# Performance work log

Measured on AMD Instinct MI355X. Metric: run time of the kernel, lower is better.

The kernel has to match this reference:

```python
import jax, jax.numpy as jnp
import numpy as np

B, C, N = 2, 512, 2048
HEADS, DIM_HEAD, SCALE = 16, 64, 8.0
H_DIM = HEADS * DIM_HEAD
EPS = 1e-12  # F.normalize default eps


def setup_inputs() -> dict:
    key = jax.random.key(0)
    ks = jax.random.split(key, 5)
    x = jax.random.normal(ks[0], (B, C, N), dtype=jnp.float32)
    Wqkv = jax.random.normal(ks[1], (3 * H_DIM, C), dtype=jnp.float32) * (1.0 / np.sqrt(C))
    q_scale = jnp.ones((DIM_HEAD,), dtype=jnp.float32)
    k_scale = jnp.ones((DIM_HEAD,), dtype=jnp.float32)
    Wout = jax.random.normal(ks[2], (C, H_DIM), dtype=jnp.float32) * (1.0 / np.sqrt(H_DIM))
    bout = jax.random.normal(ks[3], (C,), dtype=jnp.float32) * 0.01
    return {"x": x, "Wqkv": Wqkv, "q_scale": q_scale, "k_scale": k_scale,
            "Wout": Wout, "bout": bout}


def _l2norm(t):
    # F.normalize(t, dim=-1): t / max(||t||, eps)
    n = jnp.sqrt(jnp.sum(t * t, axis=-1, keepdims=True))
    return t / jnp.maximum(n, EPS)


def reference(x, Wqkv, q_scale, k_scale, Wout, bout):
    # 1x1 conv == pointwise matmul over channel dim
    qkv = jnp.einsum('oc,bcn->bon', Wqkv, x)              # [B, 3*H_DIM, N]
    q, k, v = jnp.split(qkv, 3, axis=1)
    # unflatten channels -> [B, H, D, N]
    def to_heads(t):
        return t.reshape(B, HEADS, DIM_HEAD, N)
    q, k, v = map(to_heads, (q, k, v))
    # cosine attention: l2-normalize q,k over head dim, apply learned per-dim scales
    q = _l2norm(q.transpose(0, 1, 3, 2)) * q_scale        # [B, H, N, D]
    k = _l2norm(k.transpose(0, 1, 3, 2)) * k_scale        # [B, H, N, D]
    sim = jnp.einsum('bhid,bhjd->bhij', q, k) * SCALE     # [B, H, N, N]
    attn = jax.nn.softmax(sim, axis=-1)
    out = jnp.einsum('bhij,bhdj->bhid', attn, v)          # [B, H, N, D]
    out = out.transpose(0, 1, 3, 2).reshape(B, H_DIM, N)  # b h n d -> b (h d) n
    return jnp.einsum('oc,bcn->bon', Wout, out) + bout[None, :, None]
```

## Files before the change

kernel.cpp:

```cpp
#include <hip/hip_runtime.h>
#include <hip/hip_bf16.h>

#define BATCH 2
#define CCH   512
#define NSEQ  2048
#define HEADS 16
#define DHEAD 64
#define HDIM  1024
#define ODIM  3072
#define QK_PRESCALE 11.541560327111707f

typedef short short4v __attribute__((ext_vector_type(4)));
typedef short short8 __attribute__((ext_vector_type(8)));
typedef float float4v __attribute__((ext_vector_type(4)));
typedef int   int4v   __attribute__((ext_vector_type(4)));

__device__ __forceinline__ unsigned short f2bf(float f) {
    unsigned int u = __float_as_uint(f);
    return (unsigned short)((u + 0x7FFFu + ((u >> 16) & 1u)) >> 16);
}
__device__ __forceinline__ unsigned short f2bf_fast(float f) {
    return (unsigned short)((__float_as_uint(f) + 0x8000u) >> 16);
}
__device__ __forceinline__ float fexp2(float x) {
#if __has_builtin(__builtin_amdgcn_exp2f)
    return __builtin_amdgcn_exp2f(x);
#else
    return exp2f(x);
#endif
}
__device__ __forceinline__ int pack_bf16(float lo, float hi) {
#if __has_builtin(__builtin_amdgcn_cvt_pk_bf16_f32)
    typedef __bf16 bf2_t __attribute__((ext_vector_type(2)));
    bf2_t v = __builtin_amdgcn_cvt_pk_bf16_f32(lo, hi);
    return __builtin_bit_cast(int, v);
#else
    return (int)f2bf_fast(lo) | ((int)(unsigned)f2bf_fast(hi) << 16);
#endif
}

typedef __attribute__((address_space(1))) const void* as1_cvp;
typedef __attribute__((address_space(3))) void* as3_vp;
__device__ __forceinline__ void cp16(const void* g, void* l) {
    __builtin_amdgcn_global_load_lds((as1_cvp)g, (as3_vp)l, 16, 0, 0);
}
__global__ __launch_bounds__(256) void k_prep(
    const float* __restrict__ Wqkv, const float* __restrict__ Wout,
    const float* __restrict__ x,
    const float* __restrict__ qs, const float* __restrict__ ks,
    unsigned short* __restrict__ Wqkvb, unsigned short* __restrict__ Woutb,
    unsigned short* __restrict__ xt, float* __restrict__ M) {
    const int bx = blockIdx.x;
    if (bx < 2048) {
        if (bx == 0 && threadIdx.x < 64) {
            int lane = threadIdx.x;
            float p = fabsf(qs[lane] * ks[lane]);
#pragma unroll
            for (int off = 1; off < 64; off <<= 1) p = fmaxf(p, __shfl_xor(p, off));
            if (lane == 0) *M = QK_PRESCALE * p;
        }
        int i4 = (bx * 256 + threadIdx.x) * 4;
        const float* src; unsigned short* dst; int idx;
        if (i4 < ODIM * CCH) { src = Wqkv; dst = Wqkvb; idx = i4; }
        else { src = Wout; dst = Woutb; idx = i4 - ODIM * CCH; }
        float4 v = *(const float4*)(src + idx);
        ushort4 o;
        o.x = f2bf(v.x); o.y = f2bf(v.y); o.z = f2bf(v.z); o.w = f2bf(v.w);
        *(ushort4*)(dst + idx) = o;
        return;
    }
    __shared__ unsigned short t[64][65];
    const int fx = bx - 2048;
    const int n0 = (fx & 31) * 64;
    const int c0 = ((fx >> 5) & 7) * 64;
    const int b  = fx >> 8;
    const int tr = threadIdx.x >> 6, tc = threadIdx.x & 63;
    const float* xs = x + (size_t)b * CCH * NSEQ;
    unsigned short* xd = xt + (size_t)b * NSEQ * CCH;
#pragma unroll
    for (int r = 0; r < 16; ++r) {
        int c = r * 4 + tr;
        t[c][tc] = f2bf(xs[(size_t)(c0 + c) * NSEQ + n0 + tc]);
    }
    __syncthreads();
#pragma unroll
    for (int r = 0; r < 16; ++r) {
        int n = r * 4 + tr;
        xd[(size_t)(n0 + n) * CCH + c0 + tc] = t[tc][n];
    }
}

__global__ __launch_bounds__(256) void k_gemm_qkv(
    const unsigned short* __restrict__ W, const unsigned short* __restrict__ xt,
    const float* __restrict__ qs, const float* __restrict__ ks,
    unsigned short* __restrict__ qh, unsigned short* __restrict__ kh,
    unsigned short* __restrict__ vb) {
    constexpr int K = CCH, N = NSEQ;
    __shared__ __align__(16) short smem[2 * 2 * 128 * 32];
    const int tid = threadIdx.x, wave = tid >> 6, lane = tid & 63;
    const int l15 = lane & 15, quad = lane >> 4;
    const int n0 = blockIdx.x * 128, m0 = blockIdx.y * 128, z = blockIdx.z;
    const short* Ab = (const short*)W + (size_t)m0 * K;
    const short* Bb = (const short*)xt + ((size_t)z * N + n0) * K;
    const int wm = wave >> 1, wn = wave & 1;
    const int srow = tid >> 2;
    const int cswz2 = (((tid & 3) ^ ((srow >> 1) & 3))) * 8;
    const int rchunk = ((quad ^ ((l15 >> 1) & 3))) * 8;

    float4v acc[4][4];
#pragma unroll
    for (int i = 0; i < 4; ++i)
#pragma unroll
        for (int j = 0; j < 4; ++j) acc[i][j] = (float4v){0.f, 0.f, 0.f, 0.f};

#define STAGEQ(K0_, BUF_) do {                                                   \
        short* bA = smem + (BUF_) * 8192 + wave * 512;                           \
        cp16(Ab + (size_t)srow * K + (K0_) + cswz2, bA);                         \
        cp16(Ab + (size_t)(64 + srow) * K + (K0_) + cswz2, bA + 2048);           \
        cp16(Bb + (size_t)srow * K + (K0_) + cswz2, bA + 4096);                  \
        cp16(Bb + (size_t)(64 + srow) * K + (K0_) + cswz2, bA + 6144);           \
    } while (0)

    STAGEQ(0, 0);
    __syncthreads();
    for (int ksi = 0; ksi < K / 32; ++ksi) {
        const int rb = ksi & 1;
        if (ksi + 1 < K / 32) STAGEQ((ksi + 1) * 32, rb ^ 1);
        const short* sA = smem + rb * 8192;
        const short* sB = sA + 4096;
        short8 af[4], bfr[4];
#pragma unroll
        for (int t = 0; t < 4; ++t) {
            af[t]  = *(const short8*)&sA[(wm * 64 + t * 16 + l15) * 32 + rchunk];
            bfr[t] = *(const short8*)&sB[(wn * 64 + t * 16 + l15) * 32 + rchunk];
        }
#pragma unroll
        for (int mt = 0; mt < 4; ++mt)
#pragma unroll
            for (int nt = 0; nt < 4; ++nt)
                acc[mt][nt] = __builtin_amdgcn_mfma_f32_16x16x32_bf16(af[mt], bfr[nt], acc[mt][nt], 0, 0, 0);
        __syncthreads();
    }
#undef STAGEQ

    const int co   = (m0 + wm * 64) >> 6;
    const int part = co >> 4;
    const int h    = co & 15;
    const int bh   = z * HEADS + h;
    short* myT = smem + wave * 4096;

    if (part < 2) {
        float inv[4];
#pragma unroll
        for (int nt = 0; nt < 4; ++nt) {
            float ss = 0.f;
#pragma unroll
            for (int mt = 0; mt < 4; ++mt)
#pragma unroll
                for (int r = 0; r < 4; ++r) ss += acc[mt][nt][r] * acc[mt][nt][r];
            ss += __shfl_xor(ss, 16);
            ss += __shfl_xor(ss, 32);
            inv[nt] = 1.0f / fmaxf(sqrtf(ss), 1e-12f);
        }
        const float* sc = part ? ks : qs;
        const float csc = part ? 1.0f : QK_PRESCALE;
#pragma unroll
        for (int mt = 0; mt < 4; ++mt) {
            const int db = mt * 16 + quad * 4;
            float4 s4 = *(const float4*)(sc + db);
            s4.x *= csc; s4.y *= csc; s4.z *= csc; s4.w *= csc;
#pragma unroll
            for (int nt = 0; nt < 4; ++nt) {
                int nl = nt * 16 + l15;
                short4v o;
                o.x = (short)f2bf(acc[mt][nt][0] * inv[nt] * s4.x);
                o.y = (short)f2bf(acc[mt][nt][1] * inv[nt] * s4.y);
                o.z = (short)f2bf(acc[mt][nt][2] * inv[nt] * s4.z);
                o.w = (short)f2bf(acc[mt][nt][3] * inv[nt] * s4.w);
                *(short4v*)&myT[nl * 64 + (((db >> 3) ^ (nl & 7)) << 3) + (db & 7)] = o;
            }
        }
        unsigned short* dst = (part ? kh : qh) + (size_t)bh * NSEQ * DHEAD
                              + (size_t)(n0 + wn * 64) * DHEAD;
#pragma unroll
        for (int pass = 0; pass < 8; ++pass) {
            int nl = pass * 8 + (lane >> 3), c = lane & 7;
            short8 vv = *(const short8*)&myT[nl * 64 + ((c ^ (nl & 7)) << 3)];
            *(short8*)&dst[(size_t)nl * DHEAD + c * 8] = vv;
        }
    } else {
#pragma unroll
        for (int mt = 0; mt < 4; ++mt)
#pragma unroll
            for (int nt = 0; nt < 4; ++nt) {
                int nl = nt * 16 + l15;
                int swc = nl >> 3, swo = nl & 7;
#pragma unroll
                for (int r = 0; r < 4; ++r) {
                    int d = mt * 16 + quad * 4 + r;
                    myT[d * 64 + ((swc ^ (d & 7)) << 3) + swo] = (short)f2bf(acc[mt][nt][r]);
                }
            }
        unsigned short* dst = vb + (size_t)bh * DHEAD * NSEQ + n0 + wn * 64;
#pragma unroll
        for (int pass = 0; pass < 8; ++pass) {
            int d = pass * 8 + (lane >> 3), c = lane & 7;
            short8 vv = *(const short8*)&myT[d * 64 + ((c ^ (d & 7)) << 3)];
            *(short8*)&dst[(size_t)d * NSEQ + c * 8] = vv;
        }
    }
}

#define KVB 32
__global__ __launch_bounds__(512, 4) void k_attn(
    const unsigned short* __restrict__ qh, const unsigned short* __restrict__ kh,
    const unsigned short* __restrict__ vb,
    unsigned short* __restrict__ aot, const float* __restrict__ Mptr) {
    __shared__ __align__(16) short Kt[2][4][KVB * 64];
    __shared__ __align__(16) short Vt[2][4][64 * KVB];
    const int tid = threadIdx.x, wave = tid >> 6, lane = tid & 63;
    const int grp = wave >> 2, w4 = wave & 3;
    const int gtid = tid & 255;
    const int l15 = lane & 15, quad = lane >> 4, q8 = quad * 8;
    const int flat = blockIdx.x;
    const int xcd = flat & 7, idx = flat >> 3;
    const int bh = xcd * 4 + (idx >> 4);
    const int i0 = (idx & 15) * 128;
    const int b = bh >> 4, h = bh & 15;
    const float Ms = *Mptr;
    const float4v mInit = (float4v){-Ms, -Ms, -Ms, -Ms};
    const int srow = gtid >> 3;
    const int kkey  = (srow & 3) | (((srow >> 3) & 1) << 2);
    const int cswzK = ((gtid & 7) ^ kkey) * 8;
    const int srowV = gtid >> 2;
    const int cswzV = ((gtid & 3) ^ ((srowV >> 1) & 3)) * 8;
    const int ksw = l15 & 7;
    const int kc0 = ((0 + quad) ^ ksw) * 8;
    const int kc1 = ((4 + quad) ^ ksw) * 8;
    const int vkr = (l15 >> 1) & 3;
    const int ar0 = (l15 >> 2) * 8 + (l15 & 3);
    const int ar1 = ar0 + 4;
    const int jbase = grp * (NSEQ / 2);

    short8 qf[2][2];
    {
        const short* qb = (const short*)qh + ((size_t)bh * NSEQ + i0 + w4 * 32) * DHEAD;
#pragma unroll
        for (int it = 0; it < 2; ++it) {
            qf[it][0] = *(const short8*)&qb[(it * 16 + l15) * DHEAD + q8];
            qf[it][1] = *(const short8*)&qb[(it * 16 + l15) * DHEAD + 32 + q8];
        }
    }

    float4v of[2][4];
#pragma unroll
    for (int it = 0; it < 2; ++it)
#pragma unroll
        for (int dt = 0; dt < 4; ++dt) of[it][dt] = (float4v){0.f, 0.f, 0.f, 0.f};
    float l_acc[2] = {0.f, 0.f};

    const short* kbase = (const short*)kh + ((size_t)bh * NSEQ + jbase) * DHEAD;
    const short* vbase = (const short*)vb + (size_t)bh * DHEAD * NSEQ + jbase;

#define STAGE(T_, B_) do {                                                       \
        cp16(kbase + (size_t)((T_) * KVB + srow) * DHEAD + cswzK,                \
             &Kt[grp][B_][w4 * 512]);                                            \
        cp16(vbase + (size_t)srowV * NSEQ + (T_) * KVB + cswzV,                  \
             &Vt[grp][B_][w4 * 512]);                                            \
    } while (0)

#define COMPUTE(CB_) do {                                                        \
        const short* Kb = &Kt[grp][CB_][0];                                      \
        const short* Vb = &Vt[grp][CB_][0];                                      \
        __builtin_amdgcn_s_setprio(1);                                           \
        short8 av[4];                                                            \
        _Pragma("unroll")                                                        \
        for (int dt = 0; dt < 4; ++dt)                                           \
            av[dt] = *(const short8*)&Vb[(dt * 16 + l15) * KVB + ((quad ^ vkr) * 8)]; \
        int4v pw[2];                                                             \
        _Pragma("unroll")                                                        \
        for (int t2 = 0; t2 < 2; ++t2) {                                         \
            const int arow = t2 ? ar1 : ar0;                                     \
            const short* kr = &Kb[arow * 64];                                    \
            short8 kf0 = *(const short8*)&kr[kc0];                               \
            short8 kf1 = *(const short8*)&kr[kc1];                               \
            _Pragma("unroll")                                                    \
            for (int it = 0; it < 2; ++it) {                                     \
                float4v s = mInit;                                               \
                s = __builtin_amdgcn_mfma_f32_16x16x32_bf16(kf0, qf[it][0], s, 0, 0, 0); \
                s = __builtin_amdgcn_mfma_f32_16x16x32_bf16(kf1, qf[it][1], s, 0, 0, 0); \
                float p0 = fexp2(s[0]);                                          \
                float p1 = fexp2(s[1]);                                          \
                float p2 = fexp2(s[2]);                                          \
                float p3 = fexp2(s[3]);                                          \
                l_acc[it] += (p0 + p1) + (p2 + p3);                              \
                pw[it][t2 * 2 + 0] = pack_bf16(p0, p1);                          \
                pw[it][t2 * 2 + 1] = pack_bf16(p2, p3);                          \
            }                                                                    \
        }                                                                        \
        {                                                                        \
            short8 pb0 = __builtin_bit_cast(short8, pw[0]);                      \
            short8 pb1 = __builtin_bit_cast(short8, pw[1]);                      \
            _Pragma("unroll")                                                    \
            for (int dt = 0; dt < 4; ++dt) {                                     \
                of[0][dt] = __builtin_amdgcn_mfma_f32_16x16x32_bf16(av[dt], pb0, of[0][dt], 0, 0, 0); \
                of[1][dt] = __builtin_amdgcn_mfma_f32_16x16x32_bf16(av[dt], pb1, of[1][dt], 0, 0, 0); \
            }                                                                    \
        }                                                                        \
        __builtin_amdgcn_s_setprio(0);                                           \
    } while (0)

#define WAITBAR(N_) do {                                                         \
        asm volatile("s_waitcnt vmcnt(" #N_ ")" ::: "memory");                   \
        __builtin_amdgcn_s_barrier();                                            \
        __builtin_amdgcn_sched_barrier(0);                                       \
    } while (0)

    constexpr int T = (NSEQ / 2) / KVB;
    STAGE(0, 0);
    STAGE(1, 1);
    for (int t = 0; t < T - 2; ++t) {
        STAGE(t + 2, (t + 2) & 3);
        WAITBAR(4);
        COMPUTE(t & 3);
    }
    WAITBAR(2);
    COMPUTE((T - 2) & 3);
    WAITBAR(0);
    COMPUTE((T - 1) & 3);
#undef STAGE
#undef COMPUTE
#undef WAITBAR

    float lred[2];
#pragma unroll
    for (int it = 0; it < 2; ++it) {
        float l = l_acc[it];
        l += __shfl_xor(l, 16);
        l += __shfl_xor(l, 32);
        lred[it] = l;
    }

    __syncthreads();

    float* F = (float*)&Kt[0][0][0];
    float* L = (float*)&Vt[0][0][0];
    if (grp == 1) {
#pragma unroll
        for (int it = 0; it < 2; ++it) {
#pragma unroll
            for (int dt = 0; dt < 4; ++dt)
                *(float4v*)&F[(((w4 * 2 + it) * 4 + dt) * 64 + lane) * 4] = of[it][dt];
            L[(w4 * 2 + it) * 64 + lane] = lred[it];
        }
    }
    __syncthreads();
    if (grp == 0) {
#pragma unroll
        for (int it = 0; it < 2; ++it) {
            float lt = lred[it] + L[(w4 * 2 + it) * 64 + lane];
            float inv = 1.0f / fmaxf(lt, 1e-30f);
            unsigned short* ob = aot + ((size_t)b * NSEQ + i0 + w4 * 32 + it * 16 + l15) * HDIM + h * DHEAD;
#pragma unroll
            for (int dt = 0; dt < 4; ++dt) {
                float4v p = *(const float4v*)&F[(((w4 * 2 + it) * 4 + dt) * 64 + lane) * 4];
                ushort4 o;
                o.x = f2bf((of[it][dt][0] + p[0]) * inv);
                o.y = f2bf((of[it][dt][1] + p[1]) * inv);
                o.z = f2bf((of[it][dt][2] + p[2]) * inv);
                o.w = f2bf((of[it][dt][3] + p[3]) * inv);
                *(ushort4*)&ob[dt * 16 + quad * 4] = o;
            }
        }
    }
}

__global__ __launch_bounds__(256) void k_gemm_out(
    const unsigned short* __restrict__ W, const unsigned short* __restrict__ aot,
    const float* __restrict__ bias, float* __restrict__ out) {
    constexpr int K = HDIM, N = NSEQ, M = CCH;
    __shared__ __align__(16) short lsm[2 * 2 * 64 * 64];
    const int tid = threadIdx.x, wave = tid >> 6, lane = tid & 63;
    const int l15 = lane & 15, quad = lane >> 4;
    const int n0 = blockIdx.x * 64, m0 = blockIdx.y * 64, z = blockIdx.z;
    const short* Ab = (const short*)W + (size_t)m0 * K;
    const short* Bb = (const short*)aot + ((size_t)z * N + n0) * K;
    const int wm = wave >> 1, wn = wave & 1;
    const int srow = tid >> 3;
    const int cswz = (((tid & 7) ^ (srow & 7))) * 8;
    const int sw7 = (l15 & 7);

    float4v acc[2][2];
#pragma unroll
    for (int i = 0; i < 2; ++i)
#pragma unroll
        for (int j = 0; j < 2; ++j) acc[i][j] = (float4v){0.f, 0.f, 0.f, 0.f};

#define STAGEO(K0_, BUF_) do {                                                   \
        short* bA = lsm + (BUF_) * 8192 + wave * 512;                            \
        cp16(Ab + (size_t)srow * K + (K0_) + cswz, bA);                          \
        cp16(Ab + (size_t)(srow + 32) * K + (K0_) + cswz, bA + 2048);            \
        cp16(Bb + (size_t)srow * K + (K0_) + cswz, bA + 4096);                   \
        cp16(Bb + (size_t)(srow + 32) * K + (K0_) + cswz, bA + 6144);            \
    } while (0)

    STAGEO(0, 0);
    __syncthreads();
    for (int ksi = 0; ksi < K / 64; ++ksi) {
        const int rb = ksi & 1;
        if (ksi + 1 < K / 64) STAGEO((ksi + 1) * 64, rb ^ 1);
        const short* sA = lsm + rb * 8192;
        const short* sB = sA + 4096;
        short8 af[2][2], bfr[2][2];
#pragma unroll
        for (int t = 0; t < 2; ++t)
#pragma unroll
            for (int kk = 0; kk < 2; ++kk) {
                af[t][kk]  = *(const short8*)&sA[(wm * 32 + t * 16 + l15) * 64 + ((kk * 4 + quad) ^ sw7) * 8];
                bfr[t][kk] = *(const short8*)&sB[(wn * 32 + t * 16 + l15) * 64 + ((kk * 4 + quad) ^ sw7) * 8];
            }
#pragma unroll
        for (int mt = 0; mt < 2; ++mt)
#pragma unroll
            for (int nt = 0; nt < 2; ++nt) {
                acc[mt][nt] = __builtin_amdgcn_mfma_f32_16x16x32_bf16(af[mt][0], bfr[nt][0], acc[mt][nt], 0, 0, 0);
                acc[mt][nt] = __builtin_amdgcn_mfma_f32_16x16x32_bf16(af[mt][1], bfr[nt][1], acc[mt][nt], 0, 0, 0);
            }
        __syncthreads();
    }
#undef STAGEO
    float* Co = out + (size_t)z * M * N;
#pragma unroll
    for (int mt = 0; mt < 2; ++mt)
#pragma unroll
        for (int nt = 0; nt < 2; ++nt) {
            int mrow = m0 + wm * 32 + mt * 16 + quad * 4;
#pragma unroll
            for (int r = 0; r < 4; ++r) {
                int mr = mrow + r;
                int nc = n0 + wn * 32 + nt * 16 + l15;
                Co[(size_t)mr * N + nc] = acc[mt][nt][r] + bias[mr];
            }
        }
}

extern "C" void kernel_launch(void* const* d_in, const int* in_sizes, int n_in,
                              void* d_out, int out_size, void* d_ws, size_t ws_size,
                              hipStream_t stream) {
    const float* x = nullptr; const float* Wqkv = nullptr;
    const float* qs = nullptr; const float* ks = nullptr;
    const float* Wout = nullptr; const float* bout = nullptr;
    for (int i = 0; i < n_in; ++i) {
        switch (in_sizes[i]) {
            case BATCH * CCH * NSEQ: x    = (const float*)d_in[i]; break;
            case ODIM * CCH:         Wqkv = (const float*)d_in[i]; break;
            case CCH * HDIM:         Wout = (const float*)d_in[i]; break;
            case CCH:                bout = (const float*)d_in[i]; break;
            case DHEAD: if (!qs) qs = (const float*)d_in[i]; else ks = (const float*)d_in[i]; break;
            default: break;
        }
    }
    float* y = (float*)d_out;

    char* ws = (char*)d_ws;
    float*          Mbuf  = (float*)(ws + 0);
    unsigned short* Wqkvb = (unsigned short*)(ws + 4096);
    unsigned short* Woutb = (unsigned short*)(ws + 3149824);
    unsigned short* xt    = (unsigned short*)(ws + 4198400);
    unsigned short* qh    = (unsigned short*)(ws + 8392704);
    unsigned short* kh    = (unsigned short*)(ws + 16781312);
    unsigned short* vb    = (unsigned short*)(ws + 25169920);
    unsigned short* aot   = (unsigned short*)(ws + 33558528);

    k_prep<<<dim3(2048 + 512), 256, 0, stream>>>(Wqkv, Wout, x, qs, ks, Wqkvb, Woutb, xt, Mbuf);
    k_gemm_qkv<<<dim3(NSEQ / 128, ODIM / 128, BATCH), 256, 0, stream>>>(Wqkvb, xt, qs, ks, qh, kh, vb);
    k_attn<<<dim3(512), 512, 0, stream>>>(qh, kh, vb, aot, Mbuf);
    k_gemm_out<<<dim3(NSEQ / 64, CCH / 64, BATCH), 256, 0, stream>>>(Woutb, aot, bout, y);
}
```

Before: 142.2 us.

## Fuse all four stages into one cooperative persistent kernel with grid syncs

Replaces the four separate launches (prep, QKV GEMM, attention, output GEMM) with a single cooperative kernel of 512 blocks of 512 threads, separated by grid.sync barriers. Each block's two 256-thread halves take on the prep and GEMM tiles that previously ran as separate blocks, and the original multi-launch path is kept as a fallback if the cooperative launch fails. This removes launch gaps and per-kernel tail effects, at the cost of fixed block counts: the output GEMM uses only half the threads, and some QKV tiles sit idle in one half.

```diff
diff --git a/kernel.cpp b/kernel.cpp
--- a/kernel.cpp
+++ b/kernel.cpp
@@ -1,5 +1,8 @@
 #include <hip/hip_runtime.h>
 #include <hip/hip_bf16.h>
+#include <hip/hip_cooperative_groups.h>
+
+namespace cg = cooperative_groups;
 
 #define BATCH 2
 #define CCH   512
@@ -444,6 +447,439 @@
         }
 }
 
+__global__ __launch_bounds__(512, 4) void k_fused(
+    const float* __restrict__ Wqkv, const float* __restrict__ Wout,
+    const float* __restrict__ x,
+    const float* __restrict__ qs, const float* __restrict__ ks,
+    unsigned short* __restrict__ Wqkvb, unsigned short* __restrict__ Woutb,
+    unsigned short* __restrict__ xt, float* __restrict__ Mbuf,
+    unsigned short* __restrict__ qh, unsigned short* __restrict__ kh,
+    unsigned short* __restrict__ vb, unsigned short* __restrict__ aot,
+    const float* __restrict__ bout, float* __restrict__ y) {
+    __shared__ __align__(16) short SMEM[32768];
+    cg::grid_group grid = cg::this_grid();
+    const int tid = threadIdx.x;
+    const int rb = blockIdx.x;
+    const int hf = tid >> 8;
+    const int t256 = tid & 255;
+
+    {
+        unsigned short* tt = (unsigned short*)(SMEM + hf * 16384);
+        const int s = rb * 2 + hf;
+        for (int k = 0; k < 3; ++k) {
+            const int v = s + k * 1024;
+            const bool a = v < 2560;
+            if (a && v < 2048) {
+                if (v == 0 && t256 < 64) {
+                    int lane = t256;
+                    float p = fabsf(qs[lane] * ks[lane]);
+#pragma unroll
+                    for (int off = 1; off < 64; off <<= 1) p = fmaxf(p, __shfl_xor(p, off));
+                    if (lane == 0) *Mbuf = QK_PRESCALE * p;
+                }
+                int i4 = (v * 256 + t256) * 4;
+                const float* src; unsigned short* dst; int idx;
+                if (i4 < ODIM * CCH) { src = Wqkv; dst = Wqkvb; idx = i4; }
+                else { src = Wout; dst = Woutb; idx = i4 - ODIM * CCH; }
+                float4 vv = *(const float4*)(src + idx);
+                ushort4 o;
+                o.x = f2bf(vv.x); o.y = f2bf(vv.y); o.z = f2bf(vv.z); o.w = f2bf(vv.w);
+                *(ushort4*)(dst + idx) = o;
+            }
+            const int fx = v - 2048;
+            const int tr = t256 >> 6, tc = t256 & 63;
+            if (a && v >= 2048) {
+                const int n0 = (fx & 31) * 64;
+                const int c0 = ((fx >> 5) & 7) * 64;
+                const int b  = fx >> 8;
+                const float* xs = x + (size_t)b * CCH * NSEQ;
+#pragma unroll
+                for (int r = 0; r < 16; ++r) {
+                    int c = r * 4 + tr;
+                    tt[c * 65 + tc] = f2bf(xs[(size_t)(c0 + c) * NSEQ + n0 + tc]);
+                }
+            }
+            __syncthreads();
+            if (a && v >= 2048) {
+                const int n0 = (fx & 31) * 64;
+                const int c0 = ((fx >> 5) & 7) * 64;
+                const int b  = fx >> 8;
+                unsigned short* xd = xt + (size_t)b * NSEQ * CCH;
+#pragma unroll
+                for (int r = 0; r < 16; ++r) {
+                    int n = r * 4 + tr;
+                    xd[(size_t)(n0 + n) * CCH + c0 + tc] = tt[tc * 65 + n];
+                }
+            }
+            __syncthreads();
+        }
+    }
+    grid.sync();
+
+    {
+        const int s = rb * 2 + hf;
+        bool act; int v;
+        if (s < 512)      { act = true;  v = s; }
+        else if (hf == 0) { act = true;  v = 512 + (rb - 256); }
+        else              { act = false; v = 0; }
+        constexpr int K = CCH, N = NSEQ;
+        short* smq = SMEM + hf * 16384;
+        const int wave = t256 >> 6, lane = t256 & 63;
+        const int l15 = lane & 15, quad = lane >> 4;
+        const int z = v / 384, rr = v % 384;
+        const int m0 = (rr >> 4) * 128, n0 = (rr & 15) * 128;
+        const short* Ab = (const short*)Wqkvb + (size_t)m0 * K;
+        const short* Bb = (const short*)xt + ((size_t)z * N + n0) * K;
+        const int wm = wave >> 1, wn = wave & 1;
+        const int srow = t256 >> 2;
+        const int cswz2 = (((t256 & 3) ^ ((srow >> 1) & 3))) * 8;
+        const int rchunk = ((quad ^ ((l15 >> 1) & 3))) * 8;
+
+        float4v acc[4][4];
+#pragma unroll
+        for (int i = 0; i < 4; ++i)
+#pragma unroll
+            for (int j = 0; j < 4; ++j) acc[i][j] = (float4v){0.f, 0.f, 0.f, 0.f};
+
+#define FQ_STAGE(K0_, BUF_) do {                                                 \
+        short* bA = smq + (BUF_) * 8192 + wave * 512;                            \
+        cp16(Ab + (size_t)srow * K + (K0_) + cswz2, bA);                         \
+        cp16(Ab + (size_t)(64 + srow) * K + (K0_) + cswz2, bA + 2048);           \
+        cp16(Bb + (size_t)srow * K + (K0_) + cswz2, bA + 4096);                  \
+        cp16(Bb + (size_t)(64 + srow) * K + (K0_) + cswz2, bA + 6144);           \
+    } while (0)
+
+        if (act) FQ_STAGE(0, 0);
+        __syncthreads();
+        for (int ksi = 0; ksi < K / 32; ++ksi) {
+            if (act) {
+                const int pb = ksi & 1;
+                if (ksi + 1 < K / 32) FQ_STAGE((ksi + 1) * 32, pb ^ 1);
+                const short* sA = smq + pb * 8192;
+                const short* sB = sA + 4096;
+                short8 af[4], bfr[4];
+#pragma unroll
+                for (int t = 0; t < 4; ++t) {
+                    af[t]  = *(const short8*)&sA[(wm * 64 + t * 16 + l15) * 32 + rchunk];
+                    bfr[t] = *(const short8*)&sB[(wn * 64 + t * 16 + l15) * 32 + rchunk];
+                }
+#pragma unroll
+                for (int mt = 0; mt < 4; ++mt)
+#pragma unroll
+                    for (int nt = 0; nt < 4; ++nt)
+                        acc[mt][nt] = __builtin_amdgcn_mfma_f32_16x16x32_bf16(af[mt], bfr[nt], acc[mt][nt], 0, 0, 0);
+            }
+            __syncthreads();
+        }
+#undef FQ_STAGE
+
+        if (act) {
+            const int co   = (m0 + wm * 64) >> 6;
+            const int part = co >> 4;
+            const int h    = co & 15;
+            const int bh   = z * HEADS + h;
+            short* myT = smq + wave * 4096;
+
+            if (part < 2) {
+                float inv[4];
+#pragma unroll
+                for (int nt = 0; nt < 4; ++nt) {
+                    float ss = 0.f;
+#pragma unroll
+                    for (int mt = 0; mt < 4; ++mt)
+#pragma unroll
+                        for (int r = 0; r < 4; ++r) ss += acc[mt][nt][r] * acc[mt][nt][r];
+                    ss += __shfl_xor(ss, 16);
+                    ss += __shfl_xor(ss, 32);
+                    inv[nt] = 1.0f / fmaxf(sqrtf(ss), 1e-12f);
+                }
+                const float* sc = part ? ks : qs;
+                const float csc = part ? 1.0f : QK_PRESCALE;
+#pragma unroll
+                for (int mt = 0; mt < 4; ++mt) {
+                    const int db = mt * 16 + quad * 4;
+                    float4 s4 = *(const float4*)(sc + db);
+                    s4.x *= csc; s4.y *= csc; s4.z *= csc; s4.w *= csc;
+#pragma unroll
+                    for (int nt = 0; nt < 4; ++nt) {
+                        int nl = nt * 16 + l15;
+                        short4v o;
+                        o.x = (short)f2bf(acc[mt][nt][0] * inv[nt] * s4.x);
+                        o.y = (short)f2bf(acc[mt][nt][1] * inv[nt] * s4.y);
+                        o.z = (short)f2bf(acc[mt][nt][2] * inv[nt] * s4.z);
+                        o.w = (short)f2bf(acc[mt][nt][3] * inv[nt] * s4.w);
+                        *(short4v*)&myT[nl * 64 + (((db >> 3) ^ (nl & 7)) << 3) + (db & 7)] = o;
+                    }
+                }
+                unsigned short* dst = (part ? kh : qh) + (size_t)bh * NSEQ * DHEAD
+                                      + (size_t)(n0 + wn * 64) * DHEAD;
+#pragma unroll
+                for (int pass = 0; pass < 8; ++pass) {
+                    int nl = pass * 8 + (lane >> 3), c = lane & 7;
+                    short8 vv = *(const short8*)&myT[nl * 64 + ((c ^ (nl & 7)) << 3)];
+                    *(short8*)&dst[(size_t)nl * DHEAD + c * 8] = vv;
+                }
+            } else {
+#pragma unroll
+                for (int mt = 0; mt < 4; ++mt)
+#pragma unroll
+                    for (int nt = 0; nt < 4; ++nt) {
+                        int nl = nt * 16 + l15;
+                        int swc = nl >> 3, swo = nl & 7;
+#pragma unroll
+                        for (int r = 0; r < 4; ++r) {
+                            int d = mt * 16 + quad * 4 + r;
+                            myT[d * 64 + ((swc ^ (d & 7)) << 3) + swo] = (short)f2bf(acc[mt][nt][r]);
+                        }
+                    }
+                unsigned short* dst = vb + (size_t)bh * DHEAD * NSEQ + n0 + wn * 64;
+#pragma unroll
+                for (int pass = 0; pass < 8; ++pass) {
+                    int d = pass * 8 + (lane >> 3), c = lane & 7;
+                    short8 vv = *(const short8*)&myT[d * 64 + ((c ^ (d & 7)) << 3)];
+                    *(short8*)&dst[(size_t)d * NSEQ + c * 8] = vv;
+                }
+            }
+        }
+    }
+    grid.sync();
+
+    {
+        short (*Kt)[4][KVB * 64] = (short (*)[4][KVB * 64])SMEM;
+        short (*Vt)[4][64 * KVB] = (short (*)[4][64 * KVB])(SMEM + 16384);
+        const int wave = tid >> 6, lane = tid & 63;
+        const int grp2 = wave >> 2, w4 = wave & 3;
+        const int gtid = tid & 255;
+        const int l15 = lane & 15, quad = lane >> 4, q8 = quad * 8;
+        const int flat = rb;
+        const int xcd = flat & 7, idx = flat >> 3;
+        const int bh = xcd * 4 + (idx >> 4);
+        const int i0 = (idx & 15) * 128;
+        const int b = bh >> 4, h = bh & 15;
+        const float Ms = *Mbuf;
+        const float4v mInit = (float4v){-Ms, -Ms, -Ms, -Ms};
+        const int srow = gtid >> 3;
+        const int kkey  = (srow & 3) | (((srow >> 3) & 1) << 2);
+        const int cswzK = ((gtid & 7) ^ kkey) * 8;
+        const int srowV = gtid >> 2;
+        const int cswzV = ((gtid & 3) ^ ((srowV >> 1) & 3)) * 8;
+        const int ksw = l15 & 7;
+        const int kc0 = ((0 + quad) ^ ksw) * 8;
+        const int kc1 = ((4 + quad) ^ ksw) * 8;
+        const int vkr = (l15 >> 1) & 3;
+        const int ar0 = (l15 >> 2) * 8 + (l15 & 3);
+        const int ar1 = ar0 + 4;
+        const int jbase = grp2 * (NSEQ / 2);
+
+        short8 qf[2][2];
+        {
+            const short* qb = (const short*)qh + ((size_t)bh * NSEQ + i0 + w4 * 32) * DHEAD;
+#pragma unroll
+            for (int it = 0; it < 2; ++it) {
+                qf[it][0] = *(const short8*)&qb[(it * 16 + l15) * DHEAD + q8];
+                qf[it][1] = *(const short8*)&qb[(it * 16 + l15) * DHEAD + 32 + q8];
+            }
+        }
+
+        float4v of[2][4];
+#pragma unroll
+        for (int it = 0; it < 2; ++it)
+#pragma unroll
+            for (int dt = 0; dt < 4; ++dt) of[it][dt] = (float4v){0.f, 0.f, 0.f, 0.f};
+        float l_acc[2] = {0.f, 0.f};
+
+        const short* kbase = (const short*)kh + ((size_t)bh * NSEQ + jbase) * DHEAD;
+        const short* vbase = (const short*)vb + (size_t)bh * DHEAD * NSEQ + jbase;
+
+#define FA_STAGE(T_, B_) do {                                                    \
+        cp16(kbase + (size_t)((T_) * KVB + srow) * DHEAD + cswzK,                \
+             &Kt[grp2][B_][w4 * 512]);                                           \
+        cp16(vbase + (size_t)srowV * NSEQ + (T_) * KVB + cswzV,                  \
+             &Vt[grp2][B_][w4 * 512]);                                           \
+    } while (0)
+
+#define FA_COMPUTE(CB_) do {                                                     \
+        const short* Kb = &Kt[grp2][CB_][0];                                     \
+        const short* Vb = &Vt[grp2][CB_][0];                                     \
+        __builtin_amdgcn_s_setprio(1);                                           \
+        short8 av[4];                                                            \
+        _Pragma("unroll")                                                        \
+        for (int dt = 0; dt < 4; ++dt)                                           \
+            av[dt] = *(const short8*)&Vb[(dt * 16 + l15) * KVB + ((quad ^ vkr) * 8)]; \
+        int4v pw[2];                                                             \
+        _Pragma("unroll")                                                        \
+        for (int t2 = 0; t2 < 2; ++t2) {                                         \
+            const int arow = t2 ? ar1 : ar0;                                     \
+            const short* kr = &Kb[arow * 64];                                    \
+            short8 kf0 = *(const short8*)&kr[kc0];                               \
+            short8 kf1 = *(const short8*)&kr[kc1];                               \
+            _Pragma("unroll")                                                    \
+            for (int it = 0; it < 2; ++it) {                                     \
+                float4v s = mInit;                                               \
+                s = __builtin_amdgcn_mfma_f32_16x16x32_bf16(kf0, qf[it][0], s, 0, 0, 0); \
+                s = __builtin_amdgcn_mfma_f32_16x16x32_bf16(kf1, qf[it][1], s, 0, 0, 0); \
+                float p0 = fexp2(s[0]);                                          \
+                float p1 = fexp2(s[1]);                                          \
+                float p2 = fexp2(s[2]);                                          \
+                float p3 = fexp2(s[3]);                                          \
+                l_acc[it] += (p0 + p1) + (p2 + p3);                              \
+                pw[it][t2 * 2 + 0] = pack_bf16(p0, p1);                          \
+                pw[it][t2 * 2 + 1] = pack_bf16(p2, p3);                          \
+            }                                                                    \
+        }                                                                        \
+        {                                                                        \
+            short8 pb0 = __builtin_bit_cast(short8, pw[0]);                      \
+            short8 pb1 = __builtin_bit_cast(short8, pw[1]);                      \
+            _Pragma("unroll")                                                    \
+            for (int dt = 0; dt < 4; ++dt) {                                     \
+                of[0][dt] = __builtin_amdgcn_mfma_f32_16x16x32_bf16(av[dt], pb0, of[0][dt], 0, 0, 0); \
+                of[1][dt] = __builtin_amdgcn_mfma_f32_16x16x32_bf16(av[dt], pb1, of[1][dt], 0, 0, 0); \
+            }                                                                    \
+        }                                                                        \
+        __builtin_amdgcn_s_setprio(0);                                           \
+    } while (0)
+
+#define FA_WAITBAR(N_) do {                                                      \
+        asm volatile("s_waitcnt vmcnt(" #N_ ")" ::: "memory");                   \
+        __builtin_amdgcn_s_barrier();                                            \
+        __builtin_amdgcn_sched_barrier(0);                                       \
+    } while (0)
+
+        constexpr int T = (NSEQ / 2) / KVB;
+        FA_STAGE(0, 0);
+        FA_STAGE(1, 1);
+        for (int t = 0; t < T - 2; ++t) {
+            FA_STAGE(t + 2, (t + 2) & 3);
+            FA_WAITBAR(4);
+            FA_COMPUTE(t & 3);
+        }
+        FA_WAITBAR(2);
+        FA_COMPUTE((T - 2) & 3);
+        FA_WAITBAR(0);
+        FA_COMPUTE((T - 1) & 3);
+#undef FA_STAGE
+#undef FA_COMPUTE
+#undef FA_WAITBAR
+
+        float lred[2];
+#pragma unroll
+        for (int it = 0; it < 2; ++it) {
+            float l = l_acc[it];
+            l += __shfl_xor(l, 16);
+            l += __shfl_xor(l, 32);
+            lred[it] = l;
+        }
+
+        __syncthreads();
+
+        float* F = (float*)SMEM;
+        float* L = (float*)(SMEM + 16384);
+        if (grp2 == 1) {
+#pragma unroll
+            for (int it = 0; it < 2; ++it) {
+#pragma unroll
+                for (int dt = 0; dt < 4; ++dt)
+                    *(float4v*)&F[(((w4 * 2 + it) * 4 + dt) * 64 + lane) * 4] = of[it][dt];
+                L[(w4 * 2 + it) * 64 + lane] = lred[it];
+            }
+        }
+        __syncthreads();
+        if (grp2 == 0) {
+#pragma unroll
+            for (int it = 0; it < 2; ++it) {
+                float lt = lred[it] + L[(w4 * 2 + it) * 64 + lane];
+                float inv = 1.0f / fmaxf(lt, 1e-30f);
+                unsigned short* ob = aot + ((size_t)b * NSEQ + i0 + w4 * 32 + it * 16 + l15) * HDIM + h * DHEAD;
+#pragma unroll
+                for (int dt = 0; dt < 4; ++dt) {
+                    float4v p = *(const float4v*)&F[(((w4 * 2 + it) * 4 + dt) * 64 + lane) * 4];
+                    ushort4 o;
+                    o.x = f2bf((of[it][dt][0] + p[0]) * inv);
+                    o.y = f2bf((of[it][dt][1] + p[1]) * inv);
+                    o.z = f2bf((of[it][dt][2] + p[2]) * inv);
+                    o.w = f2bf((of[it][dt][3] + p[3]) * inv);
+                    *(ushort4*)&ob[dt * 16 + quad * 4] = o;
+                }
+            }
+        }
+    }
+    grid.sync();
+
+    {
+        const bool act = (hf == 0);
+        constexpr int K = HDIM, N = NSEQ, M = CCH;
+        short* lsm = SMEM;
+        const int wave = t256 >> 6, lane = t256 & 63;
+        const int l15 = lane & 15, quad = lane >> 4;
+        const int v = rb;
+        const int z = v >> 8, rr = v & 255;
+        const int n0 = (rr & 31) * 64, m0 = (rr >> 5) * 64;
+        const short* Ab = (const short*)Woutb + (size_t)m0 * K;
+        const short* Bb = (const short*)aot + ((size_t)z * N + n0) * K;
+        const int wm = wave >> 1, wn = wave & 1;
+        const int srow = t256 >> 3;
+        const int cswz = (((t256 & 7) ^ (srow & 7))) * 8;
+        const int sw7 = (l15 & 7);
+
+        float4v acc[2][2];
+#pragma unroll
+        for (int i = 0; i < 2; ++i)
+#pragma unroll
+            for (int j = 0; j < 2; ++j) acc[i][j] = (float4v){0.f, 0.f, 0.f, 0.f};
+
+#define FO_STAGE(K0_, BUF_) do {                                                 \
+        short* bA = lsm + (BUF_) * 8192 + wave * 512;                            \
+        cp16(Ab + (size_t)srow * K + (K0_) + cswz, bA);                          \
+        cp16(Ab + (size_t)(srow + 32) * K + (K0_) + cswz, bA + 2048);            \
+        cp16(Bb + (size_t)srow * K + (K0_) + cswz, bA + 4096);                   \
+        cp16(Bb + (size_t)(srow + 32) * K + (K0_) + cswz, bA + 6144);            \
+    } while (0)
+
+        if (act) FO_STAGE(0, 0);
+        __syncthreads();
+        for (int ksi = 0; ksi < K / 64; ++ksi) {
+            if (act) {
+                const int pb = ksi & 1;
+                if (ksi + 1 < K / 64) FO_STAGE((ksi + 1) * 64, pb ^ 1);
+                const short* sA = lsm + pb * 8192;
+                const short* sB = sA + 4096;
+                short8 af[2][2], bfr[2][2];
+#pragma unroll
+                for (int t = 0; t < 2; ++t)
+#pragma unroll
+                    for (int kk = 0; kk < 2; ++kk) {
+                        af[t][kk]  = *(const short8*)&sA[(wm * 32 + t * 16 + l15) * 64 + ((kk * 4 + quad) ^ sw7) * 8];
+                        bfr[t][kk] = *(const short8*)&sB[(wn * 32 + t * 16 + l15) * 64 + ((kk * 4 + quad) ^ sw7) * 8];
+                    }
+#pragma unroll
+                for (int mt = 0; mt < 2; ++mt)
+#pragma unroll
+                    for (int nt = 0; nt < 2; ++nt) {
+                        acc[mt][nt] = __builtin_amdgcn_mfma_f32_16x16x32_bf16(af[mt][0], bfr[nt][0], acc[mt][nt], 0, 0, 0);
+                        acc[mt][nt] = __builtin_amdgcn_mfma_f32_16x16x32_bf16(af[mt][1], bfr[nt][1], acc[mt][nt], 0, 0, 0);
+                    }
+            }
+            __syncthreads();
+        }
+#undef FO_STAGE
+        if (act) {
+            float* Co = y + (size_t)z * M * N;
+#pragma unroll
+            for (int mt = 0; mt < 2; ++mt)
+#pragma unroll
+                for (int nt = 0; nt < 2; ++nt) {
+                    int mrow = m0 + wm * 32 + mt * 16 + quad * 4;
+#pragma unroll
+                    for (int r = 0; r < 4; ++r) {
+                        int mr = mrow + r;
+                        int nc = n0 + wn * 32 + nt * 16 + l15;
+                        Co[(size_t)mr * N + nc] = acc[mt][nt][r] + bout[mr];
+                    }
+                }
+        }
+    }
+}
+
 extern "C" void kernel_launch(void* const* d_in, const int* in_sizes, int n_in,
                               void* d_out, int out_size, void* d_ws, size_t ws_size,
                               hipStream_t stream) {
@@ -472,8 +908,18 @@
     unsigned short* vb    = (unsigned short*)(ws + 25169920);
     unsigned short* aot   = (unsigned short*)(ws + 33558528);
 
-    k_prep<<<dim3(2048 + 512), 256, 0, stream>>>(Wqkv, Wout, x, qs, ks, Wqkvb, Woutb, xt, Mbuf);
-    k_gemm_qkv<<<dim3(NSEQ / 128, ODIM / 128, BATCH), 256, 0, stream>>>(Wqkvb, xt, qs, ks, qh, kh, vb);
-    k_attn<<<dim3(512), 512, 0, stream>>>(qh, kh, vb, aot, Mbuf);
-    k_gemm_out<<<dim3(NSEQ / 64, CCH / 64, BATCH), 256, 0, stream>>>(Woutb, aot, bout, y);
-}
+    void* args[] = {
+        (void*)&Wqkv, (void*)&Wout, (void*)&x, (void*)&qs, (void*)&ks,
+        (void*)&Wqkvb, (void*)&Woutb, (void*)&xt, (void*)&Mbuf,
+        (void*)&qh, (void*)&kh, (void*)&vb, (void*)&aot,
+        (void*)&bout, (void*)&y
+    };
+    hipError_t err = hipLaunchCooperativeKernel(
+        (const void*)k_fused, dim3(512), dim3(512), args, 0, stream);
+    if (err != hipSuccess) {
+        k_prep<<<dim3(2048 + 512), 256, 0, stream>>>(Wqkv, Wout, x, qs, ks, Wqkvb, Woutb, xt, Mbuf);
+        k_gemm_qkv<<<dim3(NSEQ / 128, ODIM / 128, BATCH), 256, 0, stream>>>(Wqkvb, xt, qs, ks, qh, kh, vb);
+        k_attn<<<dim3(512), 512, 0, stream>>>(qh, kh, vb, aot, Mbuf);
+        k_gemm_out<<<dim3(NSEQ / 64, CCH / 64, BATCH), 256, 0, stream>>>(Woutb, aot, bout, y);
+    }
+}
```

Result: slower. 342.4 us (+140.7%).
